# Performance work log

Measured on AMD Instinct MI355X. Metric: run time of the kernel, lower is better.

## Reference

```python
import jax, jax.numpy as jnp
import numpy as np

B, C, H, W = 8, 192, 128, 128
HEADS = 4


def setup_inputs() -> dict:
    key = jax.random.key(0)
    ks = jax.random.split(key, 5)
    s = 0.02
    x = jax.random.normal(ks[0], (B, C, H, W), dtype=jnp.float32)
    qkv_w = jax.random.normal(ks[1], (3 * C, C), dtype=jnp.float32) * s   # 1x1 conv weight
    qkv_b = jnp.zeros((3 * C,), dtype=jnp.float32)
    dw_w = jax.random.normal(ks[2], (3 * C, 1, 3, 3), dtype=jnp.float32) * s  # depthwise 3x3
    dw_b = jnp.zeros((3 * C,), dtype=jnp.float32)
    temperature = jnp.ones((HEADS, 1, 1), dtype=jnp.float32)
    proj_w = jax.random.normal(ks[3], (C, C), dtype=jnp.float32) * s      # 1x1 conv weight
    proj_b = jnp.zeros((C,), dtype=jnp.float32)
    return {"x": x, "qkv_w": qkv_w, "qkv_b": qkv_b, "dw_w": dw_w,
            "dw_b": dw_b, "temperature": temperature, "proj_w": proj_w,
            "proj_b": proj_b}


def _l2norm(t):
    # matches F.normalize(t, dim=-1): t / max(||t||_2, 1e-12)
    n = jnp.sqrt(jnp.sum(t * t, axis=-1, keepdims=True))
    return t / jnp.maximum(n, 1e-12)


def reference(x, qkv_w, qkv_b, dw_w, dw_b, temperature, proj_w, proj_b):
    b, c, h, w = x.shape
    d = c // HEADS
    # 1x1 conv -> [B, 3C, H, W]
    qkv = jnp.einsum('oc,bchw->bohw', qkv_w, x) + qkv_b[None, :, None, None]
    # depthwise 3x3 conv (groups = 3C), padding=1
    qkv = jax.lax.conv_general_dilated(
        qkv, dw_w, window_strides=(1, 1), padding=((1, 1), (1, 1)),
        dimension_numbers=('NCHW', 'OIHW', 'NCHW'),
        feature_group_count=3 * c) + dw_b[None, :, None, None]
    q, k, v = jnp.split(qkv, 3, axis=1)
    hw = h * w
    q = _l2norm(q.reshape(b, HEADS, d, hw))
    k = _l2norm(k.reshape(b, HEADS, d, hw))
    v = v.reshape(b, HEADS, d, hw)
    # transposed attention: [B, heads, d, d]
    attn = jnp.einsum('bhdn,bhen->bhde', q, k) * temperature[None]
    attn = jax.nn.softmax(attn, axis=-1)
    out = jnp.einsum('bhde,bhen->bhdn', attn, v).reshape(b, c, h, w)
    return jnp.einsum('oc,bchw->bohw', proj_w, out) + proj_b[None, :, None, None]
```

## Files before the change

kernel.cpp:

```cpp
#include <hip/hip_runtime.h>
#include <hip/hip_bf16.h>

typedef __hip_bfloat16 bf16;

#define B_   8
#define C_   192
#define OC3  576
#define H_   128
#define W_   128
#define HW_  16384
#define HEADS_ 4
#define D_   48

typedef float f32x4 __attribute__((ext_vector_type(4)));
typedef __bf16 bf16x8 __attribute__((ext_vector_type(8)));
typedef __bf16 bf16x4 __attribute__((ext_vector_type(4)));

__device__ __forceinline__ float b2f(bf16 v) { return __bfloat162float(v); }

__device__ __forceinline__ void stv4(bf16* p, const f32x4& v, float bi) {
    bf16x4 o;
#pragma unroll
    for (int r = 0; r < 4; ++r) o[r] = (__bf16)(v[r] + bi);
    *reinterpret_cast<bf16x4*>(p) = o;
}
__device__ __forceinline__ void stv4(float* p, const f32x4& v, float bi) {
    f32x4 o;
#pragma unroll
    for (int r = 0; r < 4; ++r) o[r] = v[r] + bi;
    *reinterpret_cast<f32x4*>(p) = o;
}

__device__ __forceinline__ void llds16(const void* g, void* l) {
    __builtin_amdgcn_global_load_lds(
        (const __attribute__((address_space(1))) unsigned int*)g,
        (__attribute__((address_space(3))) unsigned int*)l, 16, 0, 0);
}

__global__ void cvt_w(const float* __restrict__ qkv_w, __bf16* __restrict__ Wq) {
    const int row = blockIdx.x, c = threadIdx.x;
    Wq[row * C_ + c] = (__bf16)qkv_w[row * C_ + c];
}

__global__ void tx_cvt(const float* __restrict__ x, __bf16* __restrict__ Xt) {
    const int p0 = blockIdx.x * 128;
    const int b  = blockIdx.z;
    __shared__ __bf16 LT[128 * 196];

    for (int idx = threadIdx.x; idx < C_ * 128; idx += 256) {
        int c = idx >> 7, pp = idx & 127;
        LT[pp * 196 + c] = (__bf16)x[((size_t)b * C_ + c) * HW_ + p0 + pp];
    }
    __syncthreads();
    for (int idx = threadIdx.x; idx < 128 * 48; idx += 256) {
        int pp = idx / 48, c4 = idx % 48;
        *(uint2*)&Xt[((size_t)b * HW_ + p0 + pp) * C_ + c4 * 4] =
            *(const uint2*)&LT[pp * 196 + c4 * 4];
    }
}

__global__ void vtx(const bf16* __restrict__ qkv2, __bf16* __restrict__ vt) {
    const int p0 = blockIdx.x * 128;
    const int b  = blockIdx.z;
    const bf16* vb = qkv2 + ((size_t)b * OC3 + 384) * HW_;
    __shared__ __bf16 LT[128 * 200];

    for (int idx = threadIdx.x; idx < C_ * 128; idx += 256) {
        int c = idx >> 7, pp = idx & 127;
        LT[pp * 200 + c] = *(const __bf16*)&vb[(size_t)c * HW_ + p0 + pp];
    }
    __syncthreads();
    for (int idx = threadIdx.x; idx < 128 * 48; idx += 256) {
        int pp = idx / 48, c4 = idx % 48;
        *(uint2*)&vt[((size_t)b * HW_ + p0 + pp) * C_ + c4 * 4] =
            *(const uint2*)&LT[pp * 200 + c4 * 4];
    }
}

template<typename TOut, int KK>
__global__ __launch_bounds__(512, 4) void mfma_gemm(
        const __bf16* __restrict__ Wp, const __bf16* __restrict__ Xt,
        const float* __restrict__ bias, TOut* __restrict__ Y,
        const int O, const size_t a_bstride) {
    const int tid  = threadIdx.x;
    const int wid  = tid >> 6, lane = tid & 63;
    const int lm   = lane & 15, qd = lane >> 4;
    const int p0   = blockIdx.x * 256;
    const int o0   = blockIdx.y * 128;
    const int b    = blockIdx.z;
    const int wo0  = (wid >> 2) * 64;
    const int wn0  = (wid & 3) * 64;

    const __bf16* Wb = Wp + a_bstride * b + (size_t)o0 * KK;
    const __bf16* Xb = Xt + ((size_t)b * HW_ + p0) * KK;

    __shared__ __bf16 As[3][4096];
    __shared__ __bf16 Bs[3][8192];

    f32x4 acc[4][4] = {};

    auto stage = [&](int buf, int t) {
        const int k0 = t * 32;
        {
            const int row = tid >> 2, cslot = tid & 3;
            const int k8  = cslot ^ ((row >> 1) & 3);
            llds16(Wb + (size_t)row * KK + k0 + k8 * 8,
                   &As[buf][(size_t)(wid * 64) * 8]);
        }
#pragma unroll
        for (int r = 0; r < 2; ++r) {
            const int slot = r * 512 + tid;
            const int row  = slot >> 2, cslot = slot & 3;
            const int k8   = cslot ^ ((row >> 1) & 3);
            llds16(Xb + (size_t)row * KK + k0 + k8 * 8,
                   &Bs[buf][(size_t)(r * 512 + wid * 64) * 8]);
        }
    };

    constexpr int NT = KK >> 5;

    stage(0, 0);
    stage(1, 1);

    const int csl = qd ^ ((lm >> 1) & 3);

#pragma unroll
    for (int t = 0; t < NT; ++t) {
        __builtin_amdgcn_sched_barrier(0);
        if (t < NT - 1) asm volatile("s_waitcnt vmcnt(3)" ::: "memory");
        else            asm volatile("s_waitcnt vmcnt(0)" ::: "memory");
        __builtin_amdgcn_s_barrier();
        __builtin_amdgcn_sched_barrier(0);

        if (t + 2 < NT) stage((t + 2) % 3, t + 2);

        const int cur = t % 3;
        bf16x8 af[4], bfr[4];
#pragma unroll
        for (int i = 0; i < 4; ++i)
            af[i] = *(const bf16x8*)&As[cur][((wo0 + i * 16 + lm) * 4 + csl) * 8];
#pragma unroll
        for (int j = 0; j < 4; ++j)
            bfr[j] = *(const bf16x8*)&Bs[cur][((wn0 + j * 16 + lm) * 4 + csl) * 8];
#pragma unroll
        for (int i = 0; i < 4; ++i)
#pragma unroll
            for (int j = 0; j < 4; ++j)
                acc[i][j] = __builtin_amdgcn_mfma_f32_16x16x32_bf16(
                    bfr[j], af[i], acc[i][j], 0, 0, 0);
    }

    TOut* Yb = Y + (size_t)b * O * HW_;
#pragma unroll
    for (int i = 0; i < 4; ++i) {
        const int o = o0 + wo0 + i * 16 + lm;
        if (o < O) {
            const float bi = bias[o];
#pragma unroll
            for (int j = 0; j < 4; ++j) {
                const int p = p0 + wn0 + j * 16 + qd * 4;
                stv4(&Yb[(size_t)o * HW_ + p], acc[i][j], bi);
            }
        }
    }
}

__device__ __forceinline__ void dw_load_row(const __bf16* plane, int yy, int x0,
                                            float* r) {
    if (yy < 0 || yy > 127) {
#pragma unroll
        for (int i = 0; i < 10; ++i) r[i] = 0.f;
        return;
    }
    const __bf16* row = plane + yy * 128;
    bf16x8 v = *(const bf16x8*)(row + x0);
    r[0] = (x0 > 0) ? (float)row[x0 - 1] : 0.f;
#pragma unroll
    for (int i = 0; i < 8; ++i) r[1 + i] = (float)v[i];
    r[9] = (x0 + 8 < 128) ? (float)row[x0 + 8] : 0.f;
}

__global__ __launch_bounds__(256) void dwconv_fused(
        const bf16* __restrict__ in, const float* __restrict__ w9,
        const float* __restrict__ bias, bf16* __restrict__ out,
        float* __restrict__ sumsq) {
    const int ch = blockIdx.x;
    const int b  = blockIdx.y;
    const int tid = threadIdx.x;
    const char* ib = (const char*)(in + ((size_t)b * OC3 + ch) * HW_);

    __shared__ __bf16 plane[16384];
    __shared__ float red[256];

    {
        const int wid = tid >> 6, lane = tid & 63;
        char* lbase = (char*)plane + wid * 8192;
        const char* gbase = ib + wid * 8192;
#pragma unroll
        for (int i = 0; i < 8; ++i)
            llds16(gbase + i * 1024 + lane * 16, lbase + i * 1024);
    }

    float wv[9];
#pragma unroll
    for (int i = 0; i < 9; ++i) wv[i] = w9[ch * 9 + i];
    const float bi = bias[ch];

    __syncthreads();

    const int x0 = (tid & 15) * 8;
    const int y0 = (tid >> 4) * 8;
    bf16* ob = out + ((size_t)b * OC3 + ch) * HW_;

    float rows[3][10];
    dw_load_row(plane, y0 - 1, x0, rows[0]);
    dw_load_row(plane, y0,     x0, rows[1]);

    float ss = 0.f;
#pragma unroll
    for (int yi = 0; yi < 8; ++yi) {
        float* r0 = rows[yi % 3];
        float* r1 = rows[(yi + 1) % 3];
        float* r2 = rows[(yi + 2) % 3];
        dw_load_row(plane, y0 + yi + 1, x0, r2);
        bf16x8 st;
#pragma unroll
        for (int xx = 0; xx < 8; ++xx) {
            float o = bi;
#pragma unroll
            for (int dx = 0; dx < 3; ++dx) {
                o += wv[0 + dx] * r0[xx + dx];
                o += wv[3 + dx] * r1[xx + dx];
                o += wv[6 + dx] * r2[xx + dx];
            }
            ss += o * o;
            st[xx] = (__bf16)o;
        }
        *(bf16x8*)(ob + (y0 + yi) * 128 + x0) = st;
    }

    if (ch < 384) {
        red[tid] = ss;
        __syncthreads();
        for (int stx = 128; stx > 0; stx >>= 1) {
            if (tid < stx) red[tid] += red[tid + stx];
            __syncthreads();
        }
        if (tid == 0) sumsq[b * OC3 + ch] = red[0];
    }
}

__global__ __launch_bounds__(256) void qk_mfma(const bf16* __restrict__ qkv2,
                                               float* __restrict__ Spart) {
    const int slice = blockIdx.x, h = blockIdx.y, b = blockIdx.z;
    const __bf16* qb = (const __bf16*)(qkv2 + ((size_t)b * OC3 + h * D_) * HW_);
    const __bf16* kb = (const __bf16*)(qkv2 + ((size_t)b * OC3 + 192 + h * D_) * HW_);

    __shared__ char smem[36864];
    __bf16* qs = (__bf16*)smem;
    __bf16* ks = (__bf16*)(smem + 13056);
    float*  red = (float*)smem;

    const int tid = threadIdx.x, wid = tid >> 6, lane = tid & 63;
    const int lm = lane & 15, qd = lane >> 4;
    const int kw0 = wid * 32;

    f32x4 acc[3][3] = {};

    for (int sub = 0; sub < 4; ++sub) {
        const int n0 = slice * 512 + sub * 128;
        __syncthreads();
        for (int t = tid; t < 768; t += 256) {
            int r = t >> 4, c8 = t & 15;
            *(bf16x8*)&qs[r * 136 + c8 * 8] =
                *(const bf16x8*)(qb + (size_t)r * HW_ + n0 + c8 * 8);
            *(bf16x8*)&ks[r * 136 + c8 * 8] =
                *(const bf16x8*)(kb + (size_t)r * HW_ + n0 + c8 * 8);
        }
        __syncthreads();

        bf16x8 af[3], bfr[3];
#pragma unroll
        for (int i = 0; i < 3; ++i)
            af[i] = *(const bf16x8*)&qs[(i * 16 + lm) * 136 + kw0 + qd * 8];
#pragma unroll
        for (int j = 0; j < 3; ++j)
            bfr[j] = *(const bf16x8*)&ks[(j * 16 + lm) * 136 + kw0 + qd * 8];
#pragma unroll
        for (int i = 0; i < 3; ++i)
#pragma unroll
            for (int j = 0; j < 3; ++j)
                acc[i][j] = __builtin_amdgcn_mfma_f32_16x16x32_bf16(
                    af[i], bfr[j], acc[i][j], 0, 0, 0);
    }

    __syncthreads();
    float* wb = red + wid * 2304;
#pragma unroll
    for (int i = 0; i < 3; ++i)
#pragma unroll
        for (int j = 0; j < 3; ++j)
#pragma unroll
            for (int r = 0; r < 4; ++r)
                wb[(i * 16 + qd * 4 + r) * 48 + j * 16 + lm] = acc[i][j][r];
    __syncthreads();

    float* outp = Spart + ((size_t)((b * HEADS_ + h) * 32 + slice)) * 2304;
    for (int t = tid; t < 2304; t += 256)
        outp[t] = red[t] + red[2304 + t] + red[4608 + t] + red[6912 + t];
}

__global__ void sreduce(const float* __restrict__ Spart, float* __restrict__ Sred) {
    const int bh = blockIdx.y;
    const int t  = blockIdx.x * 256 + threadIdx.x;
    const float* Sp = Spart + (size_t)bh * 32 * 2304;
    float v = 0.f;
#pragma unroll
    for (int sl = 0; sl < 32; ++sl) v += Sp[sl * 2304 + t];
    Sred[(size_t)bh * 2304 + t] = v;
}

__global__ void softmax48(const float* __restrict__ Sred, const float* __restrict__ sumsq,
                          const float* __restrict__ temp, float* __restrict__ A) {
    const int h = blockIdx.x, b = blockIdx.y;
    const int i = threadIdx.x;
    if (i >= 48) return;
    const float* sq = sumsq + b * OC3 + h * D_;
    const float* sk = sumsq + b * OC3 + 192 + h * D_;
    const float t = temp[h];
    const float* Sp = Sred + (size_t)(b * HEADS_ + h) * 2304;

    const float rqi = 1.0f / fmaxf(sqrtf(sq[i]), 1e-12f);

    float s[48];
#pragma unroll
    for (int j = 0; j < 48; ++j)
        s[j] = Sp[i * 48 + j] * rqi * (1.0f / fmaxf(sqrtf(sk[j]), 1e-12f)) * t;
    float m = -1e30f;
#pragma unroll
    for (int j = 0; j < 48; ++j) m = fmaxf(m, s[j]);
    float sum = 0.f;
#pragma unroll
    for (int j = 0; j < 48; ++j) { s[j] = expf(s[j] - m); sum += s[j]; }
    float inv = 1.0f / sum;
    float* Ao = A + ((size_t)(b * HEADS_ + h) * 48 + i) * 48;
#pragma unroll
    for (int j = 0; j < 48; ++j) Ao[j] = s[j] * inv;
}

__global__ void wfuse(const float* __restrict__ proj_w, const float* __restrict__ A,
                      __bf16* __restrict__ Wf) {
    const int o = blockIdx.x, b = blockIdx.y;
    const int cp = threadIdx.x;
    const int h = cp / 48, j = cp % 48;
    const float* wrow = proj_w + o * C_ + h * D_;
    const float* Ah = A + (size_t)(b * HEADS_ + h) * 2304;
    float s = 0.f;
#pragma unroll
    for (int i = 0; i < 48; ++i) s += wrow[i] * Ah[i * 48 + j];
    Wf[((size_t)b * 256 + o) * C_ + cp] = (__bf16)s;
}

extern "C" void kernel_launch(void* const* d_in, const int* in_sizes, int n_in,
                              void* d_out, int out_size, void* d_ws, size_t ws_size,
                              hipStream_t stream) {
    const float* x      = (const float*)d_in[0];
    const float* qkv_w  = (const float*)d_in[1];
    const float* qkv_b  = (const float*)d_in[2];
    const float* dw_w   = (const float*)d_in[3];
    const float* dw_b   = (const float*)d_in[4];
    const float* temp   = (const float*)d_in[5];
    const float* proj_w = (const float*)d_in[6];
    const float* proj_b = (const float*)d_in[7];
    float* out = (float*)d_out;

    char* ws = (char*)d_ws;
    const size_t XT_BYTES  = (size_t)B_ * HW_ * C_ * 2;
    const size_t WQ_BYTES  = 640 * C_ * 2;
    const size_t WF_BYTES  = (size_t)B_ * 256 * C_ * 2;
    const size_t QKV_BYTES = (size_t)B_ * OC3 * HW_ * 2;

    size_t off = 0;
    __bf16* Xt    = (__bf16*)(ws + off); off += XT_BYTES;
    __bf16* Wq    = (__bf16*)(ws + off); off += WQ_BYTES;
    __bf16* Wf    = (__bf16*)(ws + off); off += WF_BYTES;
    bf16*   bufA  = (bf16*)(ws + off);   off += QKV_BYTES;
    bf16*   bufB  = (bf16*)(ws + off);   off += QKV_BYTES;
    float*  sumsq = (float*)(ws + off);  off += OC3 * B_ * 4;
    float*  Spart = (float*)(ws + off);  off += (size_t)32 * 2304 * 4 * 32;
    float*  Sred  = (float*)(ws + off);  off += (size_t)32 * 2304 * 4;
    float*  Attn  = (float*)(ws + off);  off += 294912;
    __bf16* vt    = Xt;

    cvt_w<<<dim3(OC3), 192, 0, stream>>>(qkv_w, Wq);

    tx_cvt<<<dim3(HW_ / 128, 1, B_), 256, 0, stream>>>(x, Xt);

    mfma_gemm<bf16, C_><<<dim3(HW_ / 256, 5, B_), 512, 0, stream>>>(
        Wq, Xt, qkv_b, bufA, OC3, 0);

    dwconv_fused<<<dim3(OC3, B_), 256, 0, stream>>>(bufA, dw_w, dw_b, bufB, sumsq);

    qk_mfma<<<dim3(32, HEADS_, B_), 256, 0, stream>>>(bufB, Spart);

    sreduce<<<dim3(9, 32), 256, 0, stream>>>(Spart, Sred);

    softmax48<<<dim3(HEADS_, B_), 64, 0, stream>>>(Sred, sumsq, temp, Attn);

    vtx<<<dim3(HW_ / 128, 1, B_), 256, 0, stream>>>(bufB, vt);

    wfuse<<<dim3(C_, B_), 192, 0, stream>>>(proj_w, Attn, Wf);

    mfma_gemm<float, C_><<<dim3(HW_ / 256, 2, B_), 512, 0, stream>>>(
        Wf, vt, proj_b, out, C_, (size_t)256 * C_);
}
```

Measured before the change: 395.5 us.

## Fuse input transposes into GEMM B-tile loading via register staging

Removes the separate tx_cvt and vtx transpose kernels. The GEMM now reads the channel-major activation directly: each thread does strided per-channel loads into registers, converts to bf16 and writes swizzled into LDS, with B double-buffered through registers. This saves a full write and re-read of the transposed activations. In exchange, B loads become strided scalar gathers, eight separate 4-byte or 2-byte loads HW apart, instead of 16-byte direct-to-LDS loads, and there are extra vmcnt(0) waits each K step.

```diff
diff --git a/kernel.cpp b/kernel.cpp
--- a/kernel.cpp
+++ b/kernel.cpp
@@ -37,51 +37,44 @@
         (__attribute__((address_space(3))) unsigned int*)l, 16, 0, 0);
 }
 
+template<typename TIn> struct BRaw;
+template<> struct BRaw<float> {
+    float v[8];
+    __device__ __forceinline__ void load(const float* __restrict__ g) {
+#pragma unroll
+        for (int j = 0; j < 8; ++j) v[j] = g[(size_t)j * HW_];
+    }
+    __device__ __forceinline__ bf16x8 pack() const {
+        bf16x8 o;
+#pragma unroll
+        for (int j = 0; j < 8; ++j) o[j] = (__bf16)v[j];
+        return o;
+    }
+};
+template<> struct BRaw<__bf16> {
+    __bf16 v[8];
+    __device__ __forceinline__ void load(const __bf16* __restrict__ g) {
+#pragma unroll
+        for (int j = 0; j < 8; ++j) v[j] = g[(size_t)j * HW_];
+    }
+    __device__ __forceinline__ bf16x8 pack() const {
+        bf16x8 o;
+#pragma unroll
+        for (int j = 0; j < 8; ++j) o[j] = v[j];
+        return o;
+    }
+};
+
 __global__ void cvt_w(const float* __restrict__ qkv_w, __bf16* __restrict__ Wq) {
     const int row = blockIdx.x, c = threadIdx.x;
     Wq[row * C_ + c] = (__bf16)qkv_w[row * C_ + c];
 }
 
-__global__ void tx_cvt(const float* __restrict__ x, __bf16* __restrict__ Xt) {
-    const int p0 = blockIdx.x * 128;
-    const int b  = blockIdx.z;
-    __shared__ __bf16 LT[128 * 196];
-
-    for (int idx = threadIdx.x; idx < C_ * 128; idx += 256) {
-        int c = idx >> 7, pp = idx & 127;
-        LT[pp * 196 + c] = (__bf16)x[((size_t)b * C_ + c) * HW_ + p0 + pp];
-    }
-    __syncthreads();
-    for (int idx = threadIdx.x; idx < 128 * 48; idx += 256) {
-        int pp = idx / 48, c4 = idx % 48;
-        *(uint2*)&Xt[((size_t)b * HW_ + p0 + pp) * C_ + c4 * 4] =
-            *(const uint2*)&LT[pp * 196 + c4 * 4];
-    }
-}
-
-__global__ void vtx(const bf16* __restrict__ qkv2, __bf16* __restrict__ vt) {
-    const int p0 = blockIdx.x * 128;
-    const int b  = blockIdx.z;
-    const bf16* vb = qkv2 + ((size_t)b * OC3 + 384) * HW_;
-    __shared__ __bf16 LT[128 * 200];
-
-    for (int idx = threadIdx.x; idx < C_ * 128; idx += 256) {
-        int c = idx >> 7, pp = idx & 127;
-        LT[pp * 200 + c] = *(const __bf16*)&vb[(size_t)c * HW_ + p0 + pp];
-    }
-    __syncthreads();
-    for (int idx = threadIdx.x; idx < 128 * 48; idx += 256) {
-        int pp = idx / 48, c4 = idx % 48;
-        *(uint2*)&vt[((size_t)b * HW_ + p0 + pp) * C_ + c4 * 4] =
-            *(const uint2*)&LT[pp * 200 + c4 * 4];
-    }
-}
-
-template<typename TOut, int KK>
+template<typename TIn, typename TOut, int KK>
 __global__ __launch_bounds__(512, 4) void mfma_gemm(
-        const __bf16* __restrict__ Wp, const __bf16* __restrict__ Xt,
+        const __bf16* __restrict__ Wp, const TIn* __restrict__ Xsrc,
         const float* __restrict__ bias, TOut* __restrict__ Y,
-        const int O, const size_t a_bstride) {
+        const int O, const size_t a_bstride, const size_t x_bstride) {
     const int tid  = threadIdx.x;
     const int wid  = tid >> 6, lane = tid & 63;
     const int lm   = lane & 15, qd = lane >> 4;
@@ -92,62 +85,74 @@
     const int wn0  = (wid & 3) * 64;
 
     const __bf16* Wb = Wp + a_bstride * b + (size_t)o0 * KK;
-    const __bf16* Xb = Xt + ((size_t)b * HW_ + p0) * KK;
+    const TIn*    Xb = Xsrc + x_bstride * b + p0;
 
     __shared__ __bf16 As[3][4096];
-    __shared__ __bf16 Bs[3][8192];
+    __shared__ __bf16 Bs[2][8192];
 
     f32x4 acc[4][4] = {};
-
-    auto stage = [&](int buf, int t) {
+    BRaw<TIn> rb[2];
+
+    const int s0o = tid,       p_0 = s0o >> 2, cs0 = s0o & 3;
+    const int s1o = 512 + tid, p_1 = s1o >> 2, cs1 = s1o & 3;
+    const int k80 = cs0 ^ ((p_0 >> 1) & 3);
+    const int k81 = cs1 ^ ((p_1 >> 1) & 3);
+
+    auto ldB = [&](int t) {
         const int k0 = t * 32;
-        {
-            const int row = tid >> 2, cslot = tid & 3;
-            const int k8  = cslot ^ ((row >> 1) & 3);
-            llds16(Wb + (size_t)row * KK + k0 + k8 * 8,
-                   &As[buf][(size_t)(wid * 64) * 8]);
-        }
-#pragma unroll
-        for (int r = 0; r < 2; ++r) {
-            const int slot = r * 512 + tid;
-            const int row  = slot >> 2, cslot = slot & 3;
-            const int k8   = cslot ^ ((row >> 1) & 3);
-            llds16(Xb + (size_t)row * KK + k0 + k8 * 8,
-                   &Bs[buf][(size_t)(r * 512 + wid * 64) * 8]);
-        }
+        rb[0].load(Xb + (size_t)(k0 + k80 * 8) * HW_ + p_0);
+        rb[1].load(Xb + (size_t)(k0 + k81 * 8) * HW_ + p_1);
     };
+    auto wrB = [&](int buf) {
+        *(bf16x8*)&Bs[buf][(size_t)s0o * 8] = rb[0].pack();
+        *(bf16x8*)&Bs[buf][(size_t)s1o * 8] = rb[1].pack();
+    };
+    auto ldA = [&](int buf, int t) {
+        const int k0 = t * 32;
+        const int row = tid >> 2, cslot = tid & 3;
+        const int k8  = cslot ^ ((row >> 1) & 3);
+        llds16(Wb + (size_t)row * KK + k0 + k8 * 8,
+               &As[buf][(size_t)(wid * 64) * 8]);
+    };
 
     constexpr int NT = KK >> 5;
 
-    stage(0, 0);
-    stage(1, 1);
+    ldB(0); ldA(0, 0);
+    asm volatile("s_waitcnt vmcnt(0)" ::: "memory");
+    wrB(0);
+    ldB(1); ldA(1, 1);
+    asm volatile("s_waitcnt lgkmcnt(0)" ::: "memory");
+    __builtin_amdgcn_s_barrier();
+    __builtin_amdgcn_sched_barrier(0);
 
     const int csl = qd ^ ((lm >> 1) & 3);
 
 #pragma unroll
     for (int t = 0; t < NT; ++t) {
-        __builtin_amdgcn_sched_barrier(0);
-        if (t < NT - 1) asm volatile("s_waitcnt vmcnt(3)" ::: "memory");
-        else            asm volatile("s_waitcnt vmcnt(0)" ::: "memory");
-        __builtin_amdgcn_s_barrier();
-        __builtin_amdgcn_sched_barrier(0);
-
-        if (t + 2 < NT) stage((t + 2) % 3, t + 2);
-
-        const int cur = t % 3;
+        const int cur2 = t & 1;
         bf16x8 af[4], bfr[4];
 #pragma unroll
         for (int i = 0; i < 4; ++i)
-            af[i] = *(const bf16x8*)&As[cur][((wo0 + i * 16 + lm) * 4 + csl) * 8];
+            af[i] = *(const bf16x8*)&As[t % 3][((wo0 + i * 16 + lm) * 4 + csl) * 8];
 #pragma unroll
         for (int j = 0; j < 4; ++j)
-            bfr[j] = *(const bf16x8*)&Bs[cur][((wn0 + j * 16 + lm) * 4 + csl) * 8];
+            bfr[j] = *(const bf16x8*)&Bs[cur2][((wn0 + j * 16 + lm) * 4 + csl) * 8];
 #pragma unroll
         for (int i = 0; i < 4; ++i)
 #pragma unroll
             for (int j = 0; j < 4; ++j)
                 acc[i][j] = __builtin_amdgcn_mfma_f32_16x16x32_bf16(
                     bfr[j], af[i], acc[i][j], 0, 0, 0);
+
+        if (t + 1 < NT) {
+            __builtin_amdgcn_sched_barrier(0);
+            asm volatile("s_waitcnt vmcnt(0)" ::: "memory");
+            wrB(cur2 ^ 1);
+            if (t + 2 < NT) { ldB(t + 2); ldA((t + 2) % 3, t + 2); }
+            asm volatile("s_waitcnt lgkmcnt(0)" ::: "memory");
+            __builtin_amdgcn_s_barrier();
+            __builtin_amdgcn_sched_barrier(0);
+        }
     }
 
     TOut* Yb = Y + (size_t)b * O * HW_;
@@ -375,13 +380,11 @@
     float* out = (float*)d_out;
 
     char* ws = (char*)d_ws;
-    const size_t XT_BYTES  = (size_t)B_ * HW_ * C_ * 2;
     const size_t WQ_BYTES  = 640 * C_ * 2;
     const size_t WF_BYTES  = (size_t)B_ * 256 * C_ * 2;
     const size_t QKV_BYTES = (size_t)B_ * OC3 * HW_ * 2;
 
     size_t off = 0;
-    __bf16* Xt    = (__bf16*)(ws + off); off += XT_BYTES;
     __bf16* Wq    = (__bf16*)(ws + off); off += WQ_BYTES;
     __bf16* Wf    = (__bf16*)(ws + off); off += WF_BYTES;
     bf16*   bufA  = (bf16*)(ws + off);   off += QKV_BYTES;
@@ -390,14 +393,11 @@
     float*  Spart = (float*)(ws + off);  off += (size_t)32 * 2304 * 4 * 32;
     float*  Sred  = (float*)(ws + off);  off += (size_t)32 * 2304 * 4;
     float*  Attn  = (float*)(ws + off);  off += 294912;
-    __bf16* vt    = Xt;
 
     cvt_w<<<dim3(OC3), 192, 0, stream>>>(qkv_w, Wq);
 
-    tx_cvt<<<dim3(HW_ / 128, 1, B_), 256, 0, stream>>>(x, Xt);
-
-    mfma_gemm<bf16, C_><<<dim3(HW_ / 256, 5, B_), 512, 0, stream>>>(
-        Wq, Xt, qkv_b, bufA, OC3, 0);
+    mfma_gemm<float, bf16, C_><<<dim3(HW_ / 256, 5, B_), 512, 0, stream>>>(
+        Wq, x, qkv_b, bufA, OC3, 0, (size_t)C_ * HW_);
 
     dwconv_fused<<<dim3(OC3, B_), 256, 0, stream>>>(bufA, dw_w, dw_b, bufB, sumsq);
 
@@ -407,10 +407,9 @@
 
     softmax48<<<dim3(HEADS_, B_), 64, 0, stream>>>(Sred, sumsq, temp, Attn);
 
-    vtx<<<dim3(HW_ / 128, 1, B_), 256, 0, stream>>>(bufB, vt);
-
     wfuse<<<dim3(C_, B_), 192, 0, stream>>>(proj_w, Attn, Wf);
 
-    mfma_gemm<float, C_><<<dim3(HW_ / 256, 2, B_), 512, 0, stream>>>(
-        Wf, vt, proj_b, out, C_, (size_t)256 * C_);
-}
+    mfma_gemm<__bf16, float, C_><<<dim3(HW_ / 256, 2, B_), 512, 0, stream>>>(
+        Wf, (const __bf16*)bufB + (size_t)384 * HW_, proj_b, out, C_,
+        (size_t)256 * C_, (size_t)OC3 * HW_);
+}
```

Measured after the change: 491.0 us. 1.24x slower.
